# Kernel optimization log

Hardware: AMD Instinct MI355X
Metric: run time of the kernel (lower is better)

The kernel has to match this reference:

```python
import jax, jax.numpy as jnp
import numpy as np

S, B, H, E, V, K, T = 256, 32, 512, 256, 10000, 3, 32
BOS, EOS = 1, 1
NEG = -1e9


def setup_inputs() -> dict:
    key = jax.random.key(0)
    ks = jax.random.split(key, 20)
    w = lambda k, sh, s=0.02: (jax.random.normal(k, sh, jnp.float32) * s)
    return {
        "encoder_states": jax.random.normal(ks[0], (S, B, H), jnp.float32),
        "last_h": jax.random.normal(ks[1], (2, B, H), jnp.float32),
        "last_c": jax.random.normal(ks[2], (2, B, H), jnp.float32),
        "attention_mask": jnp.ones((B, S), jnp.float32),
        "indices": jax.random.randint(ks[3], (B, S), 0, V),
        "emb": w(ks[4], (V, E)),
        "Wp": w(ks[5], (H, H)),        # attention: previous_state_proj
        "We": w(ks[6], (H, H)),        # attention: encoder_states_proj
        "Wv": w(ks[7], (H,)),          # attention: attention_scores_proj
        "W_ih": w(ks[8], (E + H, 4 * H)),
        "W_hh": w(ks[9], (H, 4 * H)),
        "b_ih": jnp.zeros((4 * H,), jnp.float32),
        "b_hh": jnp.zeros((4 * H,), jnp.float32),
        "Wc": w(ks[10], (E + 2 * H, V)),  # classifier
        "bc": jnp.zeros((V,), jnp.float32),
        "W_init": w(ks[11], (H, H)),   # initial_state_layer_h (used for both h and c, as in source)
        "b_init": jnp.zeros((H,), jnp.float32),
        "max_out_length": T,
    }


def reference(encoder_states, last_h, last_c, attention_mask, indices,
              emb, Wp, We, Wv, W_ih, W_hh, b_ih, b_hh, Wc, bc, W_init, b_init,
              max_out_length):
    Tlen = int(max_out_length)
    Bsz = encoder_states.shape[1]
    Vout = bc.shape[0]

    def lstm(x, h, c):
        g = x @ W_ih + b_ih + h @ W_hh + b_hh
        i, f, gg, o = jnp.split(g, 4, axis=-1)  # torch LSTMCell gate order
        c2 = jax.nn.sigmoid(f) * c + jax.nn.sigmoid(i) * jnp.tanh(gg)
        h2 = jax.nn.sigmoid(o) * jnp.tanh(c2)
        return h2, c2

    def decode_step(tok, h, c, enc, enc_proj, mask):
        ex = emb[tok]                                   # (b, E)
        pp = h @ Wp                                     # (b, H)
        sc = jnp.tanh(pp[None] + enc_proj) @ Wv         # (S, b)
        sc = jnp.where(mask.T == 0, NEG, sc)
        a = jax.nn.softmax(sc, axis=0)
        ctx = jnp.einsum('sbh,sb->bh', enc, a)          # (b, H)
        x = jnp.concatenate([ex, ctx], -1)
        h2, c2 = lstm(x, h, c)
        logits = jnp.concatenate([ex, h2, ctx], -1) @ Wc + bc
        return h2, c2, jax.nn.log_softmax(logits, -1)

    # initial decoder state: same layer applied to h and c (bug in source, replicated)
    h0 = last_h[-1] @ W_init + b_init
    c0 = last_c[-1] @ W_init + b_init
    enc_proj0 = encoder_states @ We                     # (S, B, H), precomputed once

    # --- step 0: batch-wide, then expand to beams ---
    tok0 = jnp.full((Bsz,), BOS, jnp.int32)
    h2, c2, lp = decode_step(tok0, h0, c0, encoder_states, enc_proj0, attention_mask)
    vals, idx = jax.lax.top_k(lp, K)                    # (B, K)
    tok = idx.reshape(Bsz * K).astype(jnp.int32)
    cum = vals.reshape(Bsz * K)
    eos = tok == EOS
    h = jnp.repeat(h2, K, axis=0)
    c = jnp.repeat(c2, K, axis=0)
    enc = jnp.repeat(encoder_states, K, axis=1)         # (S, B*K, H)
    enc_p = jnp.repeat(enc_proj0, K, axis=1)
    mask = jnp.repeat(attention_mask, K, axis=0)        # (B*K, S)
    preds = jnp.zeros((Tlen, Bsz * K), jnp.int32).at[0].set(tok)
    eos_only = jnp.where(jnp.arange(Vout) == EOS, 0.0, NEG)  # finished beams emit EOS for free
    batch_base = jnp.arange(Bsz)[:, None] * K

    def body(carry, t):
        h, c, tok, cum, eos, preds = carry
        h2, c2, lp = decode_step(tok, h, c, enc, enc_p, mask)
        stp = jnp.where(eos[:, None], eos_only[None], lp)
        cand = (cum[:, None] + stp).reshape(Bsz, K * Vout)
        vals, idx = jax.lax.top_k(cand, K)              # (B, K), sorted desc
        beam = idx // Vout
        ntok = (idx % Vout).astype(jnp.int32)
        g = (batch_base + beam).reshape(-1)             # global beam-reorder indices
        h = h2[g]; c = c2[g]
        tok = ntok.reshape(-1)
        cum = vals.reshape(-1)
        eos = eos[g] | (tok == EOS)
        preds = jax.lax.dynamic_update_index_in_dim(preds[:, g], tok, t, axis=0)
        return (h, c, tok, cum, eos, preds), None

    (h, c, tok, cum, eos, preds), _ = jax.lax.scan(
        body, (h, c, tok, cum, eos, preds), jnp.arange(1, Tlen))
    all_predictions = preds[:, ::K]                     # best beam per batch, (T, B)
    best_scores = cum.reshape(Bsz, K)
    return all_predictions, best_scores
```

## Files before the change

### kernel.cpp

```cpp
#include <hip/hip_runtime.h>
#include <math.h>

#define S_   256
#define B_   32
#define H_   512
#define E_   256
#define V_   10000
#define K_   3
#define T_   32
#define N1_  96
#define BOS_ 1
#define EOS_ 1
#define NEG_ (-1000000000.0f)
#define RT   4
#define LG_MT 79
#define GST  (N1_ * 4 * H_)

__global__ __launch_bounds__(256) void gemm_k(
    const float* __restrict__ A, const float* __restrict__ B1,
    const float* __restrict__ B2, int split,
    const float* __restrict__ bias1, const float* __restrict__ bias2,
    float* __restrict__ C, int N, int Kd, int M, int klen, size_t cstride)
{
  __shared__ float As[16][64];
  __shared__ float Bs[16][64];
  const int tid = threadIdx.x;
  const int m0 = blockIdx.x * 64;
  const int n0 = blockIdx.y * 64;
  const int kstart = blockIdx.z * klen;
  const int kend = kstart + klen;
  const int tm = tid & 15, tn = tid >> 4;
  const int la_n = tid & 63;
  const int la_k = (tid >> 6) * 4;
  const int lb_m = (tid & 15) * 4;
  const int lb_k = tid >> 4;

  const int an = (n0 + la_n < N) ? (n0 + la_n) : 0;
  const float* Arow = A + (size_t)an * Kd;
  float* Cpart = C + (size_t)blockIdx.z * cstride;

  float4 a_reg, b_reg;
  a_reg = *(const float4*)(Arow + kstart + la_k);
  {
    int krow = kstart + lb_k;
    const float* Brow = (krow < split) ? (B1 + (size_t)krow * M)
                                       : (B2 + (size_t)(krow - split) * M);
    int m = m0 + lb_m;
    if (m + 3 < M) b_reg = *(const float4*)(Brow + m);
    else {
      b_reg.x = (m + 0 < M) ? Brow[m + 0] : 0.f;
      b_reg.y = (m + 1 < M) ? Brow[m + 1] : 0.f;
      b_reg.z = (m + 2 < M) ? Brow[m + 2] : 0.f;
      b_reg.w = (m + 3 < M) ? Brow[m + 3] : 0.f;
    }
  }

  float acc[4][4] = {};

  for (int k0 = kstart; k0 < kend; k0 += 16) {
    if (k0 > kstart) __syncthreads();
    As[la_k + 0][la_n] = a_reg.x; As[la_k + 1][la_n] = a_reg.y;
    As[la_k + 2][la_n] = a_reg.z; As[la_k + 3][la_n] = a_reg.w;
    *(float4*)&Bs[lb_k][lb_m] = b_reg;
    __syncthreads();
    if (k0 + 16 < kend) {
      a_reg = *(const float4*)(Arow + (k0 + 16) + la_k);
      int krow = k0 + 16 + lb_k;
      const float* Brow = (krow < split) ? (B1 + (size_t)krow * M)
                                         : (B2 + (size_t)(krow - split) * M);
      int m = m0 + lb_m;
      if (m + 3 < M) b_reg = *(const float4*)(Brow + m);
      else {
        b_reg.x = (m + 0 < M) ? Brow[m + 0] : 0.f;
        b_reg.y = (m + 1 < M) ? Brow[m + 1] : 0.f;
        b_reg.z = (m + 2 < M) ? Brow[m + 2] : 0.f;
        b_reg.w = (m + 3 < M) ? Brow[m + 3] : 0.f;
      }
    }
#pragma unroll
    for (int kk = 0; kk < 16; kk++) {
      float4 av = *(const float4*)&As[kk][tn * 4];
      float4 bv = *(const float4*)&Bs[kk][tm * 4];
      float a[4] = {av.x, av.y, av.z, av.w};
      float b[4] = {bv.x, bv.y, bv.z, bv.w};
#pragma unroll
      for (int i = 0; i < 4; i++)
#pragma unroll
        for (int j = 0; j < 4; j++) acc[i][j] += a[i] * b[j];
    }
  }

  const bool addBias = (blockIdx.z == 0);
#pragma unroll
  for (int i = 0; i < 4; i++) {
    int n = n0 + tn * 4 + i;
    if (n >= N) continue;
#pragma unroll
    for (int j = 0; j < 4; j++) {
      int m = m0 + tm * 4 + j;
      if (m >= M) continue;
      float v = acc[i][j];
      if (addBias && bias1) v += bias1[m];
      if (addBias && bias2) v += bias2[m];
      Cpart[(size_t)n * M + m] = v;
    }
  }
}

__device__ __forceinline__ bool tk_better(float va, int ia, float vb, int ib) {
  return (va > vb) || (va == vb && ia < ib);
}
__device__ __forceinline__ void tk_insertN(float v, int i, float* vv, int* ii) {
  if (!tk_better(v, i, vv[RT - 1], ii[RT - 1])) return;
  vv[RT - 1] = v; ii[RT - 1] = i;
#pragma unroll
  for (int q = RT - 1; q > 0; q--) {
    if (tk_better(vv[q], ii[q], vv[q - 1], ii[q - 1])) {
      float tv = vv[q]; vv[q] = vv[q - 1]; vv[q - 1] = tv;
      int ti = ii[q]; ii[q] = ii[q - 1]; ii[q - 1] = ti;
    }
  }
}
__device__ __forceinline__ void tk_merge_reg(float* av, int* ai,
                                             const float* bv2, const int* bi2) {
  float rv[RT]; int ri[RT];
  int p = 0, q = 0;
#pragma unroll
  for (int t = 0; t < RT; t++) {
    bool ta;
    if (p >= RT) ta = false;
    else if (q >= RT) ta = true;
    else ta = tk_better(av[p], ai[p], bv2[q], bi2[q]);
    if (ta) { rv[t] = av[p]; ri[t] = ai[p]; p++; }
    else    { rv[t] = bv2[q]; ri[t] = bi2[q]; q++; }
  }
#pragma unroll
  for (int t = 0; t < RT; t++) { av[t] = rv[t]; ai[t] = ri[t]; }
}
__device__ __forceinline__ void tk_merge_lds(float* sv, int* si, int a, int b) {
  float rv[RT]; int ri[RT];
  int p = 0, q = 0;
#pragma unroll
  for (int t = 0; t < RT; t++) {
    bool ta;
    if (p >= RT) ta = false;
    else if (q >= RT) ta = true;
    else ta = tk_better(sv[a + p], si[a + p], sv[b + q], si[b + q]);
    if (ta) { rv[t] = sv[a + p]; ri[t] = si[a + p]; p++; }
    else    { rv[t] = sv[b + q]; ri[t] = si[b + q]; q++; }
  }
#pragma unroll
  for (int t = 0; t < RT; t++) { sv[a + t] = rv[t]; si[a + t] = ri[t]; }
}

__global__ __launch_bounds__(512) void lggemm_k(
    const float* __restrict__ A, const float* __restrict__ Wc,
    const float* __restrict__ bc, int Nrows,
    float* __restrict__ ptv, int* __restrict__ pti,
    float* __restrict__ pmx, float* __restrict__ psm)
{
  __shared__ float As[2][16][32];
  __shared__ float Bs[2][16][128];
  const int tid = threadIdx.x;
  const int mt = blockIdx.x;
  const int m0 = mt * 128;
  const int n0 = blockIdx.y * 32;
  const bool edge = (m0 + 128 > V_);

  if (tid < 256) {
    const int tm = tid & 31;
    const int tn = tid >> 5;
    float acc[4][4] = {};

    for (int it = 0; it < 80; it++) {
      __syncthreads();
      const int cur = it & 1;
#pragma unroll
      for (int kk = 0; kk < 16; kk++) {
        float4 av = *(const float4*)&As[cur][kk][tn * 4];
        float4 bv = *(const float4*)&Bs[cur][kk][tm * 4];
        float a[4] = {av.x, av.y, av.z, av.w};
        float b[4] = {bv.x, bv.y, bv.z, bv.w};
#pragma unroll
        for (int i = 0; i < 4; i++)
#pragma unroll
          for (int j = 0; j < 4; j++) acc[i][j] += a[i] * b[j];
      }
    }

#pragma unroll
    for (int i = 0; i < 4; i++) {
      float vv[RT]; int ii[RT];
#pragma unroll
      for (int q = 0; q < RT; q++) { vv[q] = -3.4e38f; ii[q] = 0x7fffffff; }
      float vals[4];
#pragma unroll
      for (int j = 0; j < 4; j++) {
        int m = m0 + tm * 4 + j;
        float v = (m < V_) ? (acc[i][j] + bc[m]) : -3.4e38f;
        vals[j] = v;
        if (m < V_) tk_insertN(v, m, vv, ii);
      }
#pragma unroll
      for (int off = 1; off < 32; off <<= 1) {
        float ov[RT]; int oi[RT];
#pragma unroll
        for (int q = 0; q < RT; q++) {
          ov[q] = __shfl_xor(vv[q], off);
          oi[q] = __shfl_xor(ii[q], off);
        }
        tk_merge_reg(vv, ii, ov, oi);
      }
      const float rowmax = vv[0];
      float s = 0.f;
#pragma unroll
      for (int j = 0; j < 4; j++) {
        int m = m0 + tm * 4 + j;
        if (m < V_) s += expf(vals[j] - rowmax);
      }
#pragma unroll
      for (int off = 1; off < 32; off <<= 1) s += __shfl_xor(s, off);
      const int gr = n0 + tn * 4 + i;
      if (tm == 0 && gr < Nrows) {
        const size_t pb = (size_t)gr * LG_MT + mt;
#pragma unroll
        for (int q = 0; q < RT; q++) {
          ptv[pb * RT + q] = vv[q]; pti[pb * RT + q] = ii[q];
        }
        pmx[pb] = rowmax;
        psm[pb] = s;
      }
    }
  } else {
    const int t2 = tid - 256;
    const bool aload = t2 < 128;
    const int ar = t2 & 31;
    const int ak = ((t2 >> 5) & 3) * 4;
    const int arow_idx = (n0 + ar < Nrows) ? (n0 + ar) : 0;
    const float* Arow = A + (size_t)arow_idx * 1280;

    float4 a_reg = make_float4(0.f, 0.f, 0.f, 0.f);
    float4 b_reg[2];

    if (aload) a_reg = *(const float4*)(Arow + ak);
#pragma unroll
    for (int l = 0; l < 2; l++) {
      int idx = l * 256 + t2;
      int kr = idx >> 5, c4 = (idx & 31) * 4;
      const float* Brow = Wc + (size_t)kr * V_;
      if (!edge) b_reg[l] = *(const float4*)(Brow + m0 + c4);
      else {
        float4 bv;
        bv.x = (m0 + c4 + 0 < V_) ? Brow[m0 + c4 + 0] : 0.f;
        bv.y = (m0 + c4 + 1 < V_) ? Brow[m0 + c4 + 1] : 0.f;
        bv.z = (m0 + c4 + 2 < V_) ? Brow[m0 + c4 + 2] : 0.f;
        bv.w = (m0 + c4 + 3 < V_) ? Brow[m0 + c4 + 3] : 0.f;
        b_reg[l] = bv;
      }
    }
    if (aload) {
      As[0][ak + 0][ar] = a_reg.x; As[0][ak + 1][ar] = a_reg.y;
      As[0][ak + 2][ar] = a_reg.z; As[0][ak + 3][ar] = a_reg.w;
    }
#pragma unroll
    for (int l = 0; l < 2; l++) {
      int idx = l * 256 + t2;
      int kr = idx >> 5, c4 = (idx & 31) * 4;
      *(float4*)&Bs[0][kr][c4] = b_reg[l];
    }

    for (int it = 0; it < 80; it++) {
      __syncthreads();
      if (it + 1 < 80) {
        const int kb = (it + 1) * 16;
        const int nb2 = (it + 1) & 1;
        if (aload) a_reg = *(const float4*)(Arow + kb + ak);
#pragma unroll
        for (int l = 0; l < 2; l++) {
          int idx = l * 256 + t2;
          int kr = kb + (idx >> 5), c4 = (idx & 31) * 4;
          const float* Brow = Wc + (size_t)kr * V_;
          if (!edge) b_reg[l] = *(const float4*)(Brow + m0 + c4);
          else {
            float4 bv;
            bv.x = (m0 + c4 + 0 < V_) ? Brow[m0 + c4 + 0] : 0.f;
            bv.y = (m0 + c4 + 1 < V_) ? Brow[m0 + c4 + 1] : 0.f;
            bv.z = (m0 + c4 + 2 < V_) ? Brow[m0 + c4 + 2] : 0.f;
            bv.w = (m0 + c4 + 3 < V_) ? Brow[m0 + c4 + 3] : 0.f;
            b_reg[l] = bv;
          }
        }
        if (aload) {
          As[nb2][ak + 0][ar] = a_reg.x; As[nb2][ak + 1][ar] = a_reg.y;
          As[nb2][ak + 2][ar] = a_reg.z; As[nb2][ak + 3][ar] = a_reg.w;
        }
#pragma unroll
        for (int l = 0; l < 2; l++) {
          int idx = l * 256 + t2;
          int kr = idx >> 5, c4 = (idx & 31) * 4;
          *(float4*)&Bs[nb2][kr][c4] = b_reg[l];
        }
      }
    }
  }
}

__global__ __launch_bounds__(128) void lgmerge_k(
    const float* __restrict__ ptv, const int* __restrict__ pti,
    const float* __restrict__ pmx, const float* __restrict__ psm,
    float* __restrict__ rtv, int* __restrict__ rti,
    float* __restrict__ rmax, float* __restrict__ rlse)
{
  __shared__ float sv[128 * RT];
  __shared__ int si[128 * RT];
  __shared__ float red[128];
  const int n = blockIdx.x, tid = threadIdx.x;
  float mx_t = -3.4e38f, sm_t = 0.f;
  float vv[RT]; int ii[RT];
#pragma unroll
  for (int q = 0; q < RT; q++) { vv[q] = -3.4e38f; ii[q] = 0x7fffffff; }
  if (tid < LG_MT) {
    const size_t pb = (size_t)n * LG_MT + tid;
#pragma unroll
    for (int q = 0; q < RT; q++) { vv[q] = ptv[pb * RT + q]; ii[q] = pti[pb * RT + q]; }
    mx_t = pmx[pb]; sm_t = psm[pb];
  }
#pragma unroll
  for (int q = 0; q < RT; q++) { sv[tid * RT + q] = vv[q]; si[tid * RT + q] = ii[q]; }
  __syncthreads();
  for (int st = 64; st; st >>= 1) {
    if (tid < st) tk_merge_lds(sv, si, tid * RT, (tid + st) * RT);
    __syncthreads();
  }
  red[tid] = mx_t; __syncthreads();
  for (int st = 64; st; st >>= 1) {
    if (tid < st) red[tid] = fmaxf(red[tid], red[tid + st]);
    __syncthreads();
  }
  const float Mg = red[0]; __syncthreads();
  red[tid] = sm_t * expf(mx_t - Mg); __syncthreads();
  for (int st = 64; st; st >>= 1) {
    if (tid < st) red[tid] += red[tid + st];
    __syncthreads();
  }
  if (tid < RT) { rtv[n * RT + tid] = sv[tid]; rti[n * RT + tid] = si[tid]; }
  if (tid == 0) { rmax[n] = Mg; rlse[n] = logf(red[0]); }
}

__global__ __launch_bounds__(256) void ppgemv_k(
    const float* __restrict__ h, const float* __restrict__ Wp,
    float* __restrict__ pp)
{
  __shared__ float hS[512];
  __shared__ float red[256];
  const int n = blockIdx.y, tid = threadIdx.x;
  const int m = blockIdx.x * 64 + (tid & 63);
  const int kg = tid >> 6;
  hS[tid] = h[(size_t)n * H_ + tid];
  hS[256 + tid] = h[(size_t)n * H_ + 256 + tid];
  __syncthreads();
  float acc = 0.f;
#pragma unroll 4
  for (int k = kg * 128; k < kg * 128 + 128; k++)
    acc += hS[k] * Wp[(size_t)k * H_ + m];
  red[tid] = acc;
  __syncthreads();
  if (tid < 64) {
    float v = red[tid] + red[64 + tid] + red[128 + tid] + red[192 + tid];
    pp[(size_t)n * H_ + blockIdx.x * 64 + tid] = v;
  }
}

__global__ __launch_bounds__(512) void score_k(
    const float* __restrict__ pp, const float* __restrict__ encp,
    const float* __restrict__ Wv, const float* __restrict__ mask,
    const float* __restrict__ emb, const int* __restrict__ tok,
    const float* __restrict__ h, float* __restrict__ sc,
    float* __restrict__ xcat, int bdiv, int tok_is_bos)
{
  __shared__ float ppS[512];
  __shared__ float WvS[512];
  const int n = blockIdx.y, tid = threadIdx.x;
  const int b = n / bdiv;
  ppS[tid] = pp[(size_t)n * H_ + tid];
  WvS[tid] = Wv[tid];
  if (blockIdx.x == 0) {
    xcat[(size_t)n * 1280 + E_ + H_ + tid] = h[(size_t)n * H_ + tid];
    if (tid < E_) {
      int tk = tok_is_bos ? BOS_ : tok[n];
      xcat[(size_t)n * 1280 + tid] = emb[(size_t)tk * E_ + tid];
    }
  }
  __syncthreads();
  const int w = tid >> 6, lane = tid & 63;
#pragma unroll
  for (int j = 0; j < 4; j++) {
    int s = blockIdx.x * 32 + w * 4 + j;
    const float* ep = encp + ((size_t)s * B_ + b) * H_;
    float acc = 0.f;
#pragma unroll
    for (int r = 0; r < 8; r++) {
      int hh = r * 64 + lane;
      acc += tanhf(ppS[hh] + ep[hh]) * WvS[hh];
    }
#pragma unroll
    for (int off = 32; off; off >>= 1) acc += __shfl_xor(acc, off);
    if (lane == 0)
      sc[(size_t)n * S_ + s] = (mask[(size_t)b * S_ + s] == 0.f) ? NEG_ : acc;
  }
}

__global__ __launch_bounds__(256) void ctx_k(
    const float* __restrict__ sc, const float* __restrict__ enc,
    float* __restrict__ xcat, int bdiv)
{
  __shared__ float aS[256];
  __shared__ float red[256];
  const int n = blockIdx.y, tid = threadIdx.x;
  const int b = n / bdiv;
  const int h0 = blockIdx.x * 64;
  float v = sc[(size_t)n * S_ + tid];
  red[tid] = v; __syncthreads();
  for (int st = 128; st; st >>= 1) {
    if (tid < st) red[tid] = fmaxf(red[tid], red[tid + st]);
    __syncthreads();
  }
  const float mx = red[0]; __syncthreads();
  float e = expf(v - mx);
  aS[tid] = e;
  red[tid] = e; __syncthreads();
  for (int st = 128; st; st >>= 1) {
    if (tid < st) red[tid] += red[tid + st];
    __syncthreads();
  }
  const float rsum = 1.f / red[0];
  __syncthreads();
  const int sgrp = tid >> 6, col = tid & 63;
  float acc = 0.f;
#pragma unroll 4
  for (int s0 = 0; s0 < S_; s0 += 4) {
    int s = s0 + sgrp;
    acc += aS[s] * enc[((size_t)s * B_ + b) * H_ + h0 + col];
  }
  red[tid] = acc; __syncthreads();
  if (tid < 64) {
    float total = red[tid] + red[64 + tid] + red[128 + tid] + red[192 + tid];
    xcat[(size_t)n * 1280 + E_ + h0 + tid] = total * rsum;
  }
}

__device__ __forceinline__ float sigf(float x) { return 1.f / (1.f + expf(-x)); }

__global__ __launch_bounds__(256) void lstm_k(
    const float* __restrict__ gts, const float* __restrict__ cprev,
    float* __restrict__ xcat, float* __restrict__ h2, float* __restrict__ c2)
{
  const int n = blockIdx.x, tid = threadIdx.x;
  float* xr = xcat + (size_t)n * 1280;
  for (int i = tid; i < H_; i += 256) {
    float gi = 0.f, gf = 0.f, gg = 0.f, go = 0.f;
#pragma unroll
    for (int p = 0; p < 4; p++) {
      const float* g = gts + (size_t)p * GST + (size_t)n * (4 * H_);
      gi += g[i]; gf += g[H_ + i]; gg += g[2 * H_ + i]; go += g[3 * H_ + i];
    }
    float ctx_i = xr[E_ + i];
    float cc = cprev[(size_t)n * H_ + i];
    float cv = sigf(gf) * cc + sigf(gi) * tanhf(gg);
    float hv = sigf(go) * tanhf(cv);
    c2[(size_t)n * H_ + i] = cv;
    h2[(size_t)n * H_ + i] = hv;
    xr[E_ + i] = hv;
    xr[E_ + H_ + i] = ctx_i;
  }
}

__global__ __launch_bounds__(256) void reorder0_k(
    const float* __restrict__ h2, const float* __restrict__ c2,
    float* __restrict__ h, float* __restrict__ c,
    const float* __restrict__ rtv, const int* __restrict__ rti,
    const float* __restrict__ rmax, const float* __restrict__ rlse,
    float* __restrict__ cum, int* __restrict__ eos, int* __restrict__ tok,
    int* __restrict__ preds)
{
  const int n = blockIdx.x, b = n / K_, r = n % K_, tid = threadIdx.x;
  for (int i = tid; i < H_; i += 256) {
    h[(size_t)n * H_ + i] = h2[(size_t)b * H_ + i];
    c[(size_t)n * H_ + i] = c2[(size_t)b * H_ + i];
  }
  if (tid < T_) preds[tid * N1_ + n] = 0;
  if (tid == 0) {
    float val = (rtv[b * RT + r] - rmax[b]) - rlse[b];
    int idx = rti[b * RT + r];
    preds[n] = idx;
    cum[n] = val; tok[n] = idx; eos[n] = (idx == EOS_) ? 1 : 0;
  }
}

__global__ __launch_bounds__(256) void reorder1_k(
    const float* __restrict__ h2, const float* __restrict__ c2,
    float* __restrict__ h, float* __restrict__ c,
    const float* __restrict__ rtv, const int* __restrict__ rti,
    const float* __restrict__ rmax, const float* __restrict__ rlse,
    const float* __restrict__ cumOld, float* __restrict__ cumNew,
    const int* __restrict__ eosOld, int* __restrict__ eosNew,
    const int* __restrict__ pOld, int* __restrict__ pNew,
    int* __restrict__ tok, int t)
{
  __shared__ int s_g, s_tok;
  __shared__ float s_val;
  const int n = blockIdx.x, b = n / K_, r = n % K_, tid = threadIdx.x;
  if (tid == 0) {
    float cv[3 * RT]; int cj[3 * RT]; int cnt = 0;
    for (int k = 0; k < K_; k++) {
      int row = b * K_ + k;
      float ck = cumOld[row];
      if (eosOld[row]) {
        cv[cnt] = ck; cj[cnt] = k * V_ + EOS_; cnt++;
      } else {
        float mxk = rmax[row], lsk = rlse[row];
        for (int q = 0; q < RT; q++) {
          cv[cnt] = ck + ((rtv[row * RT + q] - mxk) - lsk);
          cj[cnt] = k * V_ + rti[row * RT + q]; cnt++;
        }
      }
    }
    int used = 0, pick = -1;
    for (int rep = 0; rep <= r; rep++) {
      pick = -1;
      for (int i2 = 0; i2 < cnt; i2++) {
        if ((used >> i2) & 1) continue;
        if (pick < 0 || tk_better(cv[i2], cj[i2], cv[pick], cj[pick])) pick = i2;
      }
      used |= 1 << pick;
    }
    int j = cj[pick];
    s_val = cv[pick];
    s_g = b * K_ + j / V_;
    s_tok = j % V_;
  }
  __syncthreads();
  const int g = s_g, ntok = s_tok;
  for (int i = tid; i < H_; i += 256) {
    h[(size_t)n * H_ + i] = h2[(size_t)g * H_ + i];
    c[(size_t)n * H_ + i] = c2[(size_t)g * H_ + i];
  }
  if (tid < T_) pNew[tid * N1_ + n] = (tid == t) ? ntok : pOld[tid * N1_ + g];
  if (tid == 0) {
    cumNew[n] = s_val;
    eosNew[n] = eosOld[g] | (ntok == EOS_ ? 1 : 0);
    tok[n] = ntok;
  }
}

__global__ __launch_bounds__(256) void finalout_k(
    const int* __restrict__ preds, const float* __restrict__ cum,
    float* __restrict__ out)
{
  const int i = blockIdx.x * 256 + threadIdx.x;
  if (i < T_ * B_) {
    int t = i >> 5, b = i & 31;
    out[i] = (float)preds[t * N1_ + b * K_];
  } else if (i < T_ * B_ + N1_) {
    out[i] = cum[i - T_ * B_];
  }
}

extern "C" void kernel_launch(void* const* d_in, const int* in_sizes, int n_in,
                              void* d_out, int out_size, void* d_ws, size_t ws_size,
                              hipStream_t stream)
{
  const float* enc    = (const float*)d_in[0];
  const float* last_h = (const float*)d_in[1];
  const float* last_c = (const float*)d_in[2];
  const float* mask   = (const float*)d_in[3];
  const float* emb    = (const float*)d_in[5];
  const float* Wp     = (const float*)d_in[6];
  const float* We     = (const float*)d_in[7];
  const float* Wv     = (const float*)d_in[8];
  const float* W_ih   = (const float*)d_in[9];
  const float* W_hh   = (const float*)d_in[10];
  const float* b_ih   = (const float*)d_in[11];
  const float* b_hh   = (const float*)d_in[12];
  const float* Wc     = (const float*)d_in[13];
  const float* bc     = (const float*)d_in[14];
  const float* W_init = (const float*)d_in[15];
  const float* b_init = (const float*)d_in[16];

  float* w = (float*)d_ws;
  float* encp = w;  w += (size_t)S_ * B_ * H_;
  float* h    = w;  w += N1_ * H_;
  float* c    = w;  w += N1_ * H_;
  float* h2   = w;  w += N1_ * H_;
  float* c2   = w;  w += N1_ * H_;
  float* pp   = w;  w += N1_ * H_;
  float* sc   = w;  w += N1_ * S_;
  float* xcat = w;  w += N1_ * 1280;
  float* gts  = w;  w += 4 * GST;
  float* ptv  = w;  w += (size_t)N1_ * LG_MT * RT;
  float* pmx  = w;  w += (size_t)N1_ * LG_MT;
  float* psm  = w;  w += (size_t)N1_ * LG_MT;
  float* rtv  = w;  w += N1_ * RT;
  float* rmax = w;  w += N1_;
  float* rlse = w;  w += N1_;
  float* cumA = w;  w += N1_;
  float* cumB = w;  w += N1_;
  int* pti  = (int*)w;  w += (size_t)N1_ * LG_MT * RT;
  int* rti  = (int*)w;  w += N1_ * RT;
  int* tok  = (int*)w;  w += N1_;
  int* eosA = (int*)w;  w += N1_;
  int* eosB = (int*)w;  w += N1_;
  int* pA   = (int*)w;  w += T_ * N1_;
  int* pB   = (int*)w;  w += T_ * N1_;

  gemm_k<<<dim3(8, 1, 1), 256, 0, stream>>>(last_h + B_ * H_, W_init, nullptr, H_,
      b_init, nullptr, h, B_, H_, H_, H_, 0);
  gemm_k<<<dim3(8, 1, 1), 256, 0, stream>>>(last_c + B_ * H_, W_init, nullptr, H_,
      b_init, nullptr, c, B_, H_, H_, H_, 0);
  gemm_k<<<dim3(8, 128, 1), 256, 0, stream>>>(enc, We, nullptr, H_,
      nullptr, nullptr, encp, S_ * B_, H_, H_, H_, 0);

  for (int t = 0; t < T_; t++) {
    const int N = (t == 0) ? B_ : N1_;
    const int ntiles = (t == 0) ? 1 : 2;
    const int nt32 = (t == 0) ? 1 : 3;
    const int bdiv = (t == 0) ? 1 : K_;

    ppgemv_k<<<dim3(8, N), 256, 0, stream>>>(h, Wp, pp);
    score_k<<<dim3(8, N), 512, 0, stream>>>(pp, encp, Wv, mask, emb, tok, h,
        sc, xcat, bdiv, t == 0 ? 1 : 0);
    ctx_k<<<dim3(8, N), 256, 0, stream>>>(sc, enc, xcat, bdiv);
    gemm_k<<<dim3(32, ntiles, 4), 256, 0, stream>>>(xcat, W_ih, W_hh, E_ + H_,
        b_ih, b_hh, gts, N, 1280, 4 * H_, 320, GST);
    lstm_k<<<N, 256, 0, stream>>>(gts, c, xcat, h2, c2);
    lggemm_k<<<dim3(LG_MT, nt32), 512, 0, stream>>>(xcat, Wc, bc, N,
        ptv, pti, pmx, psm);
    lgmerge_k<<<N, 128, 0, stream>>>(ptv, pti, pmx, psm, rtv, rti, rmax, rlse);
    if (t == 0) {
      reorder0_k<<<N1_, 256, 0, stream>>>(h2, c2, h, c, rtv, rti, rmax, rlse,
          cumA, eosA, tok, pA);
    } else {
      float* cumOld = (t & 1) ? cumA : cumB;
      float* cumNew = (t & 1) ? cumB : cumA;
      int* eosOld = (t & 1) ? eosA : eosB;
      int* eosNew = (t & 1) ? eosB : eosA;
      int* pOld   = (t & 1) ? pA : pB;
      int* pNew   = (t & 1) ? pB : pA;
      reorder1_k<<<N1_, 256, 0, stream>>>(h2, c2, h, c, rtv, rti, rmax, rlse,
          cumOld, cumNew, eosOld, eosNew, pOld, pNew, tok, t);
    }
  }

  finalout_k<<<5, 256, 0, stream>>>(pB, cumB, (float*)d_out);
}
```

Baseline: 5.722 ms.

## Share encoder reads across beams and deepen logits GEMM K-tile

The attention kernels (Wp GEMV, score, context) now launch one block per batch element and handle all three beams inside it. Each encoder, encoder-projection and Wp value is loaded once and used for three accumulators instead of being fetched separately per beam. The classifier GEMM K-tile doubles from 16 to 32, halving the number of barrier iterations, and s_setprio raises compute-wave priority during the inner FMA loop. In exchange the kernels use more registers and LDS, and the attention grid has a third as many blocks.

```diff
diff --git a/kernel.cpp b/kernel.cpp
--- a/kernel.cpp
+++ b/kernel.cpp
@@ -159,8 +159,8 @@
     float* __restrict__ ptv, int* __restrict__ pti,
     float* __restrict__ pmx, float* __restrict__ psm)
 {
-  __shared__ float As[2][16][32];
-  __shared__ float Bs[2][16][128];
+  __shared__ float As[2][32][32];
+  __shared__ float Bs[2][32][128];
   const int tid = threadIdx.x;
   const int mt = blockIdx.x;
   const int m0 = mt * 128;
@@ -172,11 +172,12 @@
     const int tn = tid >> 5;
     float acc[4][4] = {};
 
-    for (int it = 0; it < 80; it++) {
+    for (int it = 0; it < 40; it++) {
       __syncthreads();
       const int cur = it & 1;
-#pragma unroll
-      for (int kk = 0; kk < 16; kk++) {
+      __builtin_amdgcn_s_setprio(1);
+#pragma unroll
+      for (int kk = 0; kk < 32; kk++) {
         float4 av = *(const float4*)&As[cur][kk][tn * 4];
         float4 bv = *(const float4*)&Bs[cur][kk][tm * 4];
         float a[4] = {av.x, av.y, av.z, av.w};
@@ -186,6 +187,7 @@
 #pragma unroll
           for (int j = 0; j < 4; j++) acc[i][j] += a[i] * b[j];
       }
+      __builtin_amdgcn_s_setprio(0);
     }
 
 #pragma unroll
@@ -233,74 +235,37 @@
     }
   } else {
     const int t2 = tid - 256;
-    const bool aload = t2 < 128;
     const int ar = t2 & 31;
-    const int ak = ((t2 >> 5) & 3) * 4;
+    const int ak = (t2 >> 5) * 4;
     const int arow_idx = (n0 + ar < Nrows) ? (n0 + ar) : 0;
     const float* Arow = A + (size_t)arow_idx * 1280;
 
-    float4 a_reg = make_float4(0.f, 0.f, 0.f, 0.f);
-    float4 b_reg[2];
-
-    if (aload) a_reg = *(const float4*)(Arow + ak);
-#pragma unroll
-    for (int l = 0; l < 2; l++) {
-      int idx = l * 256 + t2;
-      int kr = idx >> 5, c4 = (idx & 31) * 4;
-      const float* Brow = Wc + (size_t)kr * V_;
-      if (!edge) b_reg[l] = *(const float4*)(Brow + m0 + c4);
-      else {
+    auto stage = [&](int p, int buf) {
+      const int kb = p * 32;
+      float4 a_reg = *(const float4*)(Arow + kb + ak);
+      As[buf][ak + 0][ar] = a_reg.x; As[buf][ak + 1][ar] = a_reg.y;
+      As[buf][ak + 2][ar] = a_reg.z; As[buf][ak + 3][ar] = a_reg.w;
+#pragma unroll
+      for (int l = 0; l < 4; l++) {
+        const int idx = l * 256 + t2;
+        const int kr = idx >> 5, c4 = (idx & 31) * 4;
+        const float* Brow = Wc + (size_t)(kb + kr) * V_;
         float4 bv;
-        bv.x = (m0 + c4 + 0 < V_) ? Brow[m0 + c4 + 0] : 0.f;
-        bv.y = (m0 + c4 + 1 < V_) ? Brow[m0 + c4 + 1] : 0.f;
-        bv.z = (m0 + c4 + 2 < V_) ? Brow[m0 + c4 + 2] : 0.f;
-        bv.w = (m0 + c4 + 3 < V_) ? Brow[m0 + c4 + 3] : 0.f;
-        b_reg[l] = bv;
-      }
-    }
-    if (aload) {
-      As[0][ak + 0][ar] = a_reg.x; As[0][ak + 1][ar] = a_reg.y;
-      As[0][ak + 2][ar] = a_reg.z; As[0][ak + 3][ar] = a_reg.w;
-    }
-#pragma unroll
-    for (int l = 0; l < 2; l++) {
-      int idx = l * 256 + t2;
-      int kr = idx >> 5, c4 = (idx & 31) * 4;
-      *(float4*)&Bs[0][kr][c4] = b_reg[l];
-    }
-
-    for (int it = 0; it < 80; it++) {
+        if (!edge) bv = *(const float4*)(Brow + m0 + c4);
+        else {
+          bv.x = (m0 + c4 + 0 < V_) ? Brow[m0 + c4 + 0] : 0.f;
+          bv.y = (m0 + c4 + 1 < V_) ? Brow[m0 + c4 + 1] : 0.f;
+          bv.z = (m0 + c4 + 2 < V_) ? Brow[m0 + c4 + 2] : 0.f;
+          bv.w = (m0 + c4 + 3 < V_) ? Brow[m0 + c4 + 3] : 0.f;
+        }
+        *(float4*)&Bs[buf][kr][c4] = bv;
+      }
+    };
+
+    stage(0, 0);
+    for (int it = 0; it < 40; it++) {
       __syncthreads();
-      if (it + 1 < 80) {
-        const int kb = (it + 1) * 16;
-        const int nb2 = (it + 1) & 1;
-        if (aload) a_reg = *(const float4*)(Arow + kb + ak);
-#pragma unroll
-        for (int l = 0; l < 2; l++) {
-          int idx = l * 256 + t2;
-          int kr = kb + (idx >> 5), c4 = (idx & 31) * 4;
-          const float* Brow = Wc + (size_t)kr * V_;
-          if (!edge) b_reg[l] = *(const float4*)(Brow + m0 + c4);
-          else {
-            float4 bv;
-            bv.x = (m0 + c4 + 0 < V_) ? Brow[m0 + c4 + 0] : 0.f;
-            bv.y = (m0 + c4 + 1 < V_) ? Brow[m0 + c4 + 1] : 0.f;
-            bv.z = (m0 + c4 + 2 < V_) ? Brow[m0 + c4 + 2] : 0.f;
-            bv.w = (m0 + c4 + 3 < V_) ? Brow[m0 + c4 + 3] : 0.f;
-            b_reg[l] = bv;
-          }
-        }
-        if (aload) {
-          As[nb2][ak + 0][ar] = a_reg.x; As[nb2][ak + 1][ar] = a_reg.y;
-          As[nb2][ak + 2][ar] = a_reg.z; As[nb2][ak + 3][ar] = a_reg.w;
-        }
-#pragma unroll
-        for (int l = 0; l < 2; l++) {
-          int idx = l * 256 + t2;
-          int kr = idx >> 5, c4 = (idx & 31) * 4;
-          *(float4*)&Bs[nb2][kr][c4] = b_reg[l];
-        }
-      }
+      if (it + 1 < 40) stage(it + 1, (it + 1) & 1);
     }
   }
 }
@@ -349,25 +314,46 @@
 
 __global__ __launch_bounds__(256) void ppgemv_k(
     const float* __restrict__ h, const float* __restrict__ Wp,
-    float* __restrict__ pp)
-{
-  __shared__ float hS[512];
+    float* __restrict__ pp, int nbm)
+{
+  __shared__ float hS[3][512];
   __shared__ float red[256];
-  const int n = blockIdx.y, tid = threadIdx.x;
+  const int b = blockIdx.y, tid = threadIdx.x;
   const int m = blockIdx.x * 64 + (tid & 63);
   const int kg = tid >> 6;
-  hS[tid] = h[(size_t)n * H_ + tid];
-  hS[256 + tid] = h[(size_t)n * H_ + 256 + tid];
+  for (int r = 0; r < nbm; r++) {
+    hS[r][tid] = h[(size_t)(b * nbm + r) * H_ + tid];
+    hS[r][256 + tid] = h[(size_t)(b * nbm + r) * H_ + 256 + tid];
+  }
   __syncthreads();
-  float acc = 0.f;
+  if (nbm == 1) {
+    float acc = 0.f;
 #pragma unroll 4
-  for (int k = kg * 128; k < kg * 128 + 128; k++)
-    acc += hS[k] * Wp[(size_t)k * H_ + m];
-  red[tid] = acc;
-  __syncthreads();
-  if (tid < 64) {
-    float v = red[tid] + red[64 + tid] + red[128 + tid] + red[192 + tid];
-    pp[(size_t)n * H_ + blockIdx.x * 64 + tid] = v;
+    for (int k = kg * 128; k < kg * 128 + 128; k++)
+      acc += hS[0][k] * Wp[(size_t)k * H_ + m];
+    red[tid] = acc;
+    __syncthreads();
+    if (tid < 64) {
+      float v = red[tid] + red[64 + tid] + red[128 + tid] + red[192 + tid];
+      pp[(size_t)b * H_ + blockIdx.x * 64 + tid] = v;
+    }
+  } else {
+    float a0 = 0.f, a1 = 0.f, a2 = 0.f;
+#pragma unroll 4
+    for (int k = kg * 128; k < kg * 128 + 128; k++) {
+      const float wv = Wp[(size_t)k * H_ + m];
+      a0 += hS[0][k] * wv; a1 += hS[1][k] * wv; a2 += hS[2][k] * wv;
+    }
+    float av[3] = {a0, a1, a2};
+    for (int r = 0; r < 3; r++) {
+      red[tid] = av[r];
+      __syncthreads();
+      if (tid < 64) {
+        float v = red[tid] + red[64 + tid] + red[128 + tid] + red[192 + tid];
+        pp[(size_t)(b * 3 + r) * H_ + blockIdx.x * 64 + tid] = v;
+      }
+      __syncthreads();
+    }
   }
 }
 
@@ -376,19 +362,22 @@
     const float* __restrict__ Wv, const float* __restrict__ mask,
     const float* __restrict__ emb, const int* __restrict__ tok,
     const float* __restrict__ h, float* __restrict__ sc,
-    float* __restrict__ xcat, int bdiv, int tok_is_bos)
-{
-  __shared__ float ppS[512];
+    float* __restrict__ xcat, int nbm, int tok_is_bos)
+{
+  __shared__ float ppS[3][512];
   __shared__ float WvS[512];
-  const int n = blockIdx.y, tid = threadIdx.x;
-  const int b = n / bdiv;
-  ppS[tid] = pp[(size_t)n * H_ + tid];
+  const int b = blockIdx.y, tid = threadIdx.x;
+  for (int r = 0; r < nbm; r++)
+    ppS[r][tid] = pp[(size_t)(b * nbm + r) * H_ + tid];
   WvS[tid] = Wv[tid];
   if (blockIdx.x == 0) {
-    xcat[(size_t)n * 1280 + E_ + H_ + tid] = h[(size_t)n * H_ + tid];
-    if (tid < E_) {
-      int tk = tok_is_bos ? BOS_ : tok[n];
-      xcat[(size_t)n * 1280 + tid] = emb[(size_t)tk * E_ + tid];
+    for (int r = 0; r < nbm; r++) {
+      const int n = b * nbm + r;
+      xcat[(size_t)n * 1280 + E_ + H_ + tid] = h[(size_t)n * H_ + tid];
+      if (tid < E_) {
+        int tk = tok_is_bos ? BOS_ : tok[n];
+        xcat[(size_t)n * 1280 + tid] = emb[(size_t)tk * E_ + tid];
+      }
     }
   }
   __syncthreads();
@@ -397,55 +386,79 @@
   for (int j = 0; j < 4; j++) {
     int s = blockIdx.x * 32 + w * 4 + j;
     const float* ep = encp + ((size_t)s * B_ + b) * H_;
-    float acc = 0.f;
-#pragma unroll
-    for (int r = 0; r < 8; r++) {
-      int hh = r * 64 + lane;
-      acc += tanhf(ppS[hh] + ep[hh]) * WvS[hh];
-    }
-#pragma unroll
-    for (int off = 32; off; off >>= 1) acc += __shfl_xor(acc, off);
-    if (lane == 0)
-      sc[(size_t)n * S_ + s] = (mask[(size_t)b * S_ + s] == 0.f) ? NEG_ : acc;
+    float a0 = 0.f, a1 = 0.f, a2 = 0.f;
+#pragma unroll
+    for (int rr = 0; rr < 8; rr++) {
+      int hh = rr * 64 + lane;
+      const float e = ep[hh];
+      const float wvv = WvS[hh];
+      a0 += tanhf(ppS[0][hh] + e) * wvv;
+      if (nbm > 1) {
+        a1 += tanhf(ppS[1][hh] + e) * wvv;
+        a2 += tanhf(ppS[2][hh] + e) * wvv;
+      }
+    }
+#pragma unroll
+    for (int off = 32; off; off >>= 1) {
+      a0 += __shfl_xor(a0, off);
+      a1 += __shfl_xor(a1, off);
+      a2 += __shfl_xor(a2, off);
+    }
+    if (lane == 0) {
+      const bool msk = (mask[(size_t)b * S_ + s] == 0.f);
+      sc[(size_t)(b * nbm + 0) * S_ + s] = msk ? NEG_ : a0;
+      if (nbm > 1) {
+        sc[(size_t)(b * nbm + 1) * S_ + s] = msk ? NEG_ : a1;
+        sc[(size_t)(b * nbm + 2) * S_ + s] = msk ? NEG_ : a2;
+      }
+    }
   }
 }
 
 __global__ __launch_bounds__(256) void ctx_k(
     const float* __restrict__ sc, const float* __restrict__ enc,
-    float* __restrict__ xcat, int bdiv)
-{
-  __shared__ float aS[256];
+    float* __restrict__ xcat, int nbm)
+{
+  __shared__ float aS[3][256];
   __shared__ float red[256];
-  const int n = blockIdx.y, tid = threadIdx.x;
-  const int b = n / bdiv;
+  const int b = blockIdx.y, tid = threadIdx.x;
   const int h0 = blockIdx.x * 64;
-  float v = sc[(size_t)n * S_ + tid];
-  red[tid] = v; __syncthreads();
-  for (int st = 128; st; st >>= 1) {
-    if (tid < st) red[tid] = fmaxf(red[tid], red[tid + st]);
+  float rs[3];
+  for (int r = 0; r < nbm; r++) {
+    const float v = sc[(size_t)(b * nbm + r) * S_ + tid];
+    red[tid] = v; __syncthreads();
+    for (int st = 128; st; st >>= 1) {
+      if (tid < st) red[tid] = fmaxf(red[tid], red[tid + st]);
+      __syncthreads();
+    }
+    const float mx = red[0]; __syncthreads();
+    const float e = expf(v - mx);
+    aS[r][tid] = e;
+    red[tid] = e; __syncthreads();
+    for (int st = 128; st; st >>= 1) {
+      if (tid < st) red[tid] += red[tid + st];
+      __syncthreads();
+    }
+    rs[r] = 1.f / red[0];
     __syncthreads();
   }
-  const float mx = red[0]; __syncthreads();
-  float e = expf(v - mx);
-  aS[tid] = e;
-  red[tid] = e; __syncthreads();
-  for (int st = 128; st; st >>= 1) {
-    if (tid < st) red[tid] += red[tid + st];
-    __syncthreads();
-  }
-  const float rsum = 1.f / red[0];
-  __syncthreads();
   const int sgrp = tid >> 6, col = tid & 63;
-  float acc = 0.f;
+  float c0 = 0.f, c1 = 0.f, c2 = 0.f;
 #pragma unroll 4
   for (int s0 = 0; s0 < S_; s0 += 4) {
     int s = s0 + sgrp;
-    acc += aS[s] * enc[((size_t)s * B_ + b) * H_ + h0 + col];
-  }
-  red[tid] = acc; __syncthreads();
-  if (tid < 64) {
-    float total = red[tid] + red[64 + tid] + red[128 + tid] + red[192 + tid];
-    xcat[(size_t)n * 1280 + E_ + h0 + tid] = total * rsum;
+    const float ev = enc[((size_t)s * B_ + b) * H_ + h0 + col];
+    c0 += aS[0][s] * ev;
+    if (nbm > 1) { c1 += aS[1][s] * ev; c2 += aS[2][s] * ev; }
+  }
+  float cv[3] = {c0, c1, c2};
+  for (int r = 0; r < nbm; r++) {
+    red[tid] = cv[r]; __syncthreads();
+    if (tid < 64) {
+      float total = red[tid] + red[64 + tid] + red[128 + tid] + red[192 + tid];
+      xcat[(size_t)(b * nbm + r) * 1280 + E_ + h0 + tid] = total * rs[r];
+    }
+    __syncthreads();
   }
 }
 
@@ -624,12 +637,12 @@
     const int N = (t == 0) ? B_ : N1_;
     const int ntiles = (t == 0) ? 1 : 2;
     const int nt32 = (t == 0) ? 1 : 3;
-    const int bdiv = (t == 0) ? 1 : K_;
-
-    ppgemv_k<<<dim3(8, N), 256, 0, stream>>>(h, Wp, pp);
-    score_k<<<dim3(8, N), 512, 0, stream>>>(pp, encp, Wv, mask, emb, tok, h,
-        sc, xcat, bdiv, t == 0 ? 1 : 0);
-    ctx_k<<<dim3(8, N), 256, 0, stream>>>(sc, enc, xcat, bdiv);
+    const int nbm = (t == 0) ? 1 : K_;
+
+    ppgemv_k<<<dim3(8, B_), 256, 0, stream>>>(h, Wp, pp, nbm);
+    score_k<<<dim3(8, B_), 512, 0, stream>>>(pp, encp, Wv, mask, emb, tok, h,
+        sc, xcat, nbm, t == 0 ? 1 : 0);
+    ctx_k<<<dim3(8, B_), 256, 0, stream>>>(sc, enc, xcat, nbm);
     gemm_k<<<dim3(32, ntiles, 4), 256, 0, stream>>>(xcat, W_ih, W_hh, E_ + H_,
         b_ih, b_hh, gts, N, 1280, 4 * H_, 320, GST);
     lstm_k<<<N, 256, 0, stream>>>(gts, c, xcat, h2, c2);
```

Result: slower. 6.230 ms (+8.9%).
